# Performance work log

Measured on AMD Instinct MI355X. Metric: run time of the kernel, lower is better.

## Reference

```python
import jax, jax.numpy as jnp
import numpy as np

KEY_DIM, VALUE_DIM, NUM_HEAD, OUT_DIM = 128, 64, 4, 64
HEAD_KDIM = KEY_DIM // NUM_HEAD   # 32
HEAD_VDIM = VALUE_DIM // NUM_HEAD # 16

def _xavier(key, shape):
    # xavier_uniform over (fan_in=shape[0], fan_out=prod(shape[1:])) like torch
    fan_in, fan_out = shape[0], int(np.prod(shape[1:]))
    lim = float(np.sqrt(6.0 / (fan_in + fan_out)))
    return jax.random.uniform(key, shape, jnp.float32, -lim, lim)

def setup_inputs() -> dict:
    key = jax.random.key(0)
    ks = jax.random.split(key, 7)
    B, Q, K = 2, 4096, 4096
    return {
        "q_data": jax.random.normal(ks[0], (B, Q, KEY_DIM), jnp.float32),
        "m_data": jax.random.normal(ks[1], (B, K, VALUE_DIM), jnp.float32),
        "mask": jax.random.randint(ks[2], (B, K), 0, 2, jnp.int32),
        "q_weights": _xavier(ks[3], (KEY_DIM, NUM_HEAD, HEAD_KDIM)),
        "k_weights": _xavier(ks[4], (VALUE_DIM, NUM_HEAD, HEAD_KDIM)),
        "v_weights": _xavier(ks[5], (VALUE_DIM, NUM_HEAD, HEAD_VDIM)),
        "o_weights": _xavier(ks[6], (NUM_HEAD, HEAD_VDIM, OUT_DIM)),
        "o_bias": jnp.zeros((OUT_DIM,), jnp.float32),
    }

def reference(q_data, m_data, mask, q_weights, k_weights, v_weights, o_weights, o_bias):
    head_kdim = q_weights.shape[-1]
    scale = head_kdim ** (-0.5)
    Q = jnp.einsum('bqa,ahc->bqhc', q_data, q_weights) * scale
    K = jnp.einsum('bka,ahc->bkhc', m_data, k_weights)
    V = jnp.einsum('bka,ahc->bkhc', m_data, v_weights)
    logits = jnp.einsum('bqhc,bkhc->bhqk', Q, K)
    neg = jnp.finfo(logits.dtype).min
    logits = jnp.where(mask[:, None, None, :] == 0, neg, logits)
    weights = jax.nn.softmax(logits, axis=-1)
    weight_avg = jnp.einsum('bhqk,bkhc->bqhc', weights, V)
    return jnp.einsum('bqhc,hco->bqo', weight_avg, o_weights) + o_bias
```

## Files before the change

kernel.cpp:

```cpp
#include <hip/hip_runtime.h>
#include <stdint.h>

#define B_  2
#define QN  4096
#define KN  4096
#define AD  128
#define MD  64
#define H_  4
#define C_  32
#define CV  16
#define OD  64

typedef short bf16x8 __attribute__((ext_vector_type(8)));
typedef short bf16x4 __attribute__((ext_vector_type(4)));
typedef float f32x4  __attribute__((ext_vector_type(4)));

__device__ __forceinline__ short f2bf(float f) {
  union { float f; unsigned u; } v; v.f = f;
  unsigned r = v.u + 0x7fffu + ((v.u >> 16) & 1u);
  return (short)(r >> 16);
}
__device__ __forceinline__ unsigned pack2t(float a, float b) {
  union { float f; unsigned u; } ua, ub; ua.f = a; ub.f = b;
  return __builtin_amdgcn_perm(ub.u, ua.u, 0x07060302u);
}
__device__ __forceinline__ bf16x4 pack4t(f32x4 p) {
  union { unsigned u[2]; bf16x4 v; } t;
  t.u[0] = pack2t(p[0], p[1]); t.u[1] = pack2t(p[2], p[3]);
  return t.v;
}
__device__ __forceinline__ bf16x8 cvt8(f32x4 a, f32x4 b) {
  bf16x8 o;
  o[0]=f2bf(a[0]); o[1]=f2bf(a[1]); o[2]=f2bf(a[2]); o[3]=f2bf(a[3]);
  o[4]=f2bf(b[0]); o[5]=f2bf(b[1]); o[6]=f2bf(b[2]); o[7]=f2bf(b[3]);
  return o;
}

__global__ __launch_bounds__(256) void k_proj(const float* __restrict__ mdf,
                                              const float* __restrict__ kwf,
                                              const float* __restrict__ vwf,
                                              const int* __restrict__ mask, int* __restrict__ kc,
                                              short* __restrict__ Kp, short* __restrict__ Vpt) {
  __shared__ unsigned long long balS[64];
  __shared__ int pref[64];
  __shared__ int kcS;
  const int lane = threadIdx.x & 63;
  const int wid = threadIdx.x >> 6;
  const int n = lane & 15, quad = lane >> 4;
  const f32x4 z4 = {0.f,0.f,0.f,0.f};
  const int bidx = blockIdx.x;
  const int b = bidx / 768;
  #pragma unroll
  for (int p = 0; p < 16; ++p) {
    const int seg = wid*16 + p;
    const unsigned long long bal = __ballot(mask[b*KN + seg*64 + lane] != 0);
    if (lane == 0) balS[seg] = bal;
  }
  __syncthreads();
  if (wid == 0) {
    int v = __popcll(balS[lane]); int incl = v;
    for (int d = 1; d < 64; d <<= 1) { int o = __shfl_up(incl, d); if (lane >= d) incl += o; }
    pref[lane] = incl - v;
    if (lane == 63) kcS = incl;
  }
  __syncthreads();
  const int Kc = kcS;
  const int nch = (Kc + 31) >> 5;
  const int t = bidx*4 + wid;
  const int rem = t - b*3072;
  const int rt = rem / 12, ct = rem - rt*12;
  if (rem == 0 && lane == 0) kc[b] = Kc;
  if (rt*16 >= nch*32) return;
  const int j = rt*16 + n;
  const int valid = (j < Kc);
  int src = 0;
  if (valid) {
    int seg = 0;
    #pragma unroll
    for (int st = 32; st >= 1; st >>= 1)
      if (seg + st < 64 && pref[seg + st] <= j) seg += st;
    int r2 = j - pref[seg];
    unsigned long long m = balS[seg];
    int pos = 0;
    #pragma unroll
    for (int w = 32; w >= 1; w >>= 1) {
      const int c = __popcll(m & ((1ull << w) - 1ull));
      if (r2 >= c) { r2 -= c; m >>= w; pos += w; }
    }
    src = seg*64 + pos;
  }
  const float* mrow = mdf + (b*KN + src)*MD;
  const int hc = ct*16 + n;
  f32x4 acc = z4;
  #pragma unroll
  for (int ch = 0; ch < 2; ++ch) {
    const int a0 = ch*32 + quad*8;
    bf16x8 afrag = cvt8(*(const f32x4*)(mrow + a0), *(const f32x4*)(mrow + a0 + 4));
    if (!valid) {
      #pragma unroll
      for (int jj = 0; jj < 8; ++jj) afrag[jj] = 0;
    }
    bf16x8 bfrag;
    if (ct < 8) {
      #pragma unroll
      for (int jj = 0; jj < 8; ++jj) bfrag[jj] = f2bf(kwf[(a0 + jj)*128 + hc]);
    } else {
      #pragma unroll
      for (int jj = 0; jj < 8; ++jj) bfrag[jj] = f2bf(vwf[(a0 + jj)*64 + hc - 128]);
    }
    acc = __builtin_amdgcn_mfma_f32_16x16x32_bf16(afrag, bfrag, acc, 0, 0, 0);
  }
  if (ct < 8) {
    const int h = hc >> 5, c = hc & 31;
    #pragma unroll
    for (int r = 0; r < 4; ++r) {
      const int jj2 = rt*16 + quad*4 + r;
      Kp[((b*H_ + h)*KN + jj2)*C_ + c] = f2bf(acc[r]);
    }
  } else {
    const int hc2 = hc - 128; const int h = hc2 >> 4, cv = hc2 & 15;
    bf16x4 pk; pk[0]=f2bf(acc[0]); pk[1]=f2bf(acc[1]); pk[2]=f2bf(acc[2]); pk[3]=f2bf(acc[3]);
    *(bf16x4*)(Vpt + ((b*H_ + h)*CV + cv)*KN + rt*16 + quad*4) = pk;
  }
}

__global__ __launch_bounds__(1024) void k_attn(const float* __restrict__ qdf,
                                               const float* __restrict__ qwf,
                                               const short* __restrict__ Kp,
                                               const short* __restrict__ Vpt,
                                               const int* __restrict__ kc,
                                               const float* __restrict__ w2f,
                                               const float* __restrict__ obf,
                                               float* __restrict__ out) {
  __shared__ __attribute__((aligned(16))) char pool[40960];
  __shared__ __attribute__((aligned(16))) short QL[32*136];
  const int lane = threadIdx.x & 63, wid = threadIdx.x >> 6;
  const int h = wid & 3, split = wid >> 2;
  const int flatq = blockIdx.x * 32;
  const int b = flatq >> 12;
  const int bh = b*H_ + h;
  const int n = lane & 15, quad = lane >> 4;
  const int Kc = kc[b];
  const int nch = (Kc + 31) >> 5;
  const f32x4 z4 = {0.f,0.f,0.f,0.f};
  {
    const int mt = wid & 1, ct = wid >> 1;
    const int row = flatq + mt*16 + n;
    f32x4 acc = z4;
    #pragma unroll
    for (int ak = 0; ak < 4; ++ak) {
      const int a0 = ak*32 + quad*8;
      const float* ap = qdf + row*AD + a0;
      bf16x8 afrag = cvt8(*(const f32x4*)ap, *(const f32x4*)(ap + 4));
      bf16x8 bfrag;
      #pragma unroll
      for (int j = 0; j < 8; ++j) bfrag[j] = f2bf(qwf[(a0 + j)*128 + ct*16 + n]);
      acc = __builtin_amdgcn_mfma_f32_16x16x32_bf16(afrag, bfrag, acc, 0, 0, 0);
    }
    const float s = 0.17677669529663687f * 1.44269504088896341f;
    #pragma unroll
    for (int r = 0; r < 4; ++r)
      QL[(mt*16 + quad*4 + r)*136 + ct*16 + n] = f2bf(acc[r] * s);
  }
  __syncthreads();
  const bf16x8 qb0 = *(const bf16x8*)(QL + n*136 + h*32 + quad*8);
  const bf16x8 qb1 = *(const bf16x8*)(QL + (16 + n)*136 + h*32 + quad*8);
  const short* Kb = Kp + bh*KN*C_;
  const short* Vb = Vpt + bh*CV*KN;
  f32x4 o0 = z4, o1 = z4;
  float l0 = 0.f, l1 = 0.f;
  short* Pw = (short*)(pool + wid*2560);

  auto loadK = [&](int cc, bf16x8& f0, bf16x8& f1, bf16x8& v) {
    const int kb = cc*32;
    f0 = *(const bf16x8*)(Kb + (kb + n)*C_ + quad*8);
    f1 = *(const bf16x8*)(Kb + (kb + 16 + n)*C_ + quad*8);
    v  = *(const bf16x8*)(Vb + n*KN + kb + quad*8);
  };
  auto consume = [&](const bf16x8& ckf0, const bf16x8& ckf1, const bf16x8& cva) {
    f32x4 s00 = __builtin_amdgcn_mfma_f32_16x16x32_bf16(ckf0, qb0, z4, 0, 0, 0);
    f32x4 s01 = __builtin_amdgcn_mfma_f32_16x16x32_bf16(ckf0, qb1, z4, 0, 0, 0);
    f32x4 s10 = __builtin_amdgcn_mfma_f32_16x16x32_bf16(ckf1, qb0, z4, 0, 0, 0);
    f32x4 s11 = __builtin_amdgcn_mfma_f32_16x16x32_bf16(ckf1, qb1, z4, 0, 0, 0);
    f32x4 p00, p01, p10, p11;
    #pragma unroll
    for (int r = 0; r < 4; ++r) {
      p00[r] = __builtin_amdgcn_exp2f(s00[r]);
      p01[r] = __builtin_amdgcn_exp2f(s01[r]);
      p10[r] = __builtin_amdgcn_exp2f(s10[r]);
      p11[r] = __builtin_amdgcn_exp2f(s11[r]);
    }
    l0 += ((p00[0]+p00[1])+(p00[2]+p00[3])) + ((p10[0]+p10[1])+(p10[2]+p10[3]));
    l1 += ((p01[0]+p01[1])+(p01[2]+p01[3])) + ((p11[0]+p11[1])+(p11[2]+p11[3]));
    *(bf16x4*)(Pw + n*40 + quad*4)           = pack4t(p00);
    *(bf16x4*)(Pw + n*40 + 16 + quad*4)      = pack4t(p10);
    *(bf16x4*)(Pw + (16+n)*40 + quad*4)      = pack4t(p01);
    *(bf16x4*)(Pw + (16+n)*40 + 16 + quad*4) = pack4t(p11);
    const bf16x8 pb0 = *(const bf16x8*)(Pw + n*40 + quad*8);
    const bf16x8 pb1 = *(const bf16x8*)(Pw + (16+n)*40 + quad*8);
    o0 = __builtin_amdgcn_mfma_f32_16x16x32_bf16(cva, pb0, o0, 0, 0, 0);
    o1 = __builtin_amdgcn_mfma_f32_16x16x32_bf16(cva, pb1, o1, 0, 0, 0);
  };

  bf16x8 k00, k01, v0, k10, k11, v1, k20, k21, v2;
  int ci = split;
  if (ci < nch)     loadK(ci,     k00, k01, v0);
  if (ci + 4 < nch) loadK(ci + 4, k10, k11, v1);
  for (; ci < nch; ci += 12) {
    if (ci + 8 < nch) loadK(ci + 8, k20, k21, v2);
    consume(k00, k01, v0);
    if (ci + 4 < nch) {
      if (ci + 12 < nch) loadK(ci + 12, k00, k01, v0);
      consume(k10, k11, v1);
      if (ci + 8 < nch) {
        if (ci + 16 < nch) loadK(ci + 16, k10, k11, v1);
        consume(k20, k21, v2);
      }
    }
  }
  __syncthreads();
  float* Of   = (float*)pool;
  float* Lb   = (float*)(pool + 33280);
  short* ObfA = (short*)(pool + 35328);
  #pragma unroll
  for (int r = 0; r < 4; ++r) {
    const int hc = h*16 + quad*4 + r;
    Of[split*2080 + n*65 + hc]      = o0[r];
    Of[split*2080 + (16+n)*65 + hc] = o1[r];
  }
  l0 += __shfl_xor(l0, 16); l0 += __shfl_xor(l0, 32);
  l1 += __shfl_xor(l1, 16); l1 += __shfl_xor(l1, 32);
  if (lane < 16) {
    Lb[split*128 + h*32 + lane]      = l0;
    Lb[split*128 + h*32 + 16 + lane] = l1;
  }
  __syncthreads();
  {
    const float npad = (float)(nch*32 - Kc);
    const int e = threadIdx.x * 2;
    const int q = e >> 6, hc = e & 63;
    const int hh = hc >> 4;
    const float l = (Lb[hh*32 + q] + Lb[128 + hh*32 + q])
                  + (Lb[256 + hh*32 + q] + Lb[384 + hh*32 + q]) - npad;
    const float inv = 1.00135f / l;
    const float v0_ = ((Of[q*65 + hc]     + Of[2080 + q*65 + hc])
                     + (Of[4160 + q*65 + hc] + Of[6240 + q*65 + hc])) * inv;
    const float v1_ = ((Of[q*65 + hc + 1] + Of[2080 + q*65 + hc + 1])
                     + (Of[4160 + q*65 + hc + 1] + Of[6240 + q*65 + hc + 1])) * inv;
    union { unsigned u; short s[2]; } pk;
    pk.s[0] = f2bf(v0_); pk.s[1] = f2bf(v1_);
    *(unsigned*)(ObfA + q*72 + hc) = pk.u;
  }
  __syncthreads();
  if (wid < 8) {
    const int mt = wid & 1, nt = wid >> 1;
    f32x4 acc = z4;
    #pragma unroll
    for (int kchunk = 0; kchunk < 2; ++kchunk) {
      const bf16x8 afrag = *(const bf16x8*)(ObfA + (mt*16 + n)*72 + kchunk*32 + quad*8);
      bf16x8 bfrag;
      #pragma unroll
      for (int jj = 0; jj < 8; ++jj)
        bfrag[jj] = f2bf(w2f[(kchunk*32 + quad*8 + jj)*64 + nt*16 + n]);
      acc = __builtin_amdgcn_mfma_f32_16x16x32_bf16(afrag, bfrag, acc, 0, 0, 0);
    }
    const int ocol = nt*16 + n;
    const float bias = obf[ocol];
    #pragma unroll
    for (int r = 0; r < 4; ++r) {
      const int qg = flatq + mt*16 + quad*4 + r;
      out[qg*64 + ocol] = acc[r] + bias;
    }
  }
}

extern "C" void kernel_launch(void* const* d_in, const int* in_sizes, int n_in,
                              void* d_out, int out_size, void* d_ws, size_t ws_size,
                              hipStream_t stream) {
  const float* qd  = (const float*)d_in[0];
  const float* md  = (const float*)d_in[1];
  const int*   msk = (const int*)  d_in[2];
  const float* qw  = (const float*)d_in[3];
  const float* kw  = (const float*)d_in[4];
  const float* vw  = (const float*)d_in[5];
  const float* ow  = (const float*)d_in[6];
  const float* ob  = (const float*)d_in[7];
  float* out = (float*)d_out;

  char* ws = (char*)d_ws;
  int*   kc  = (int*)  (ws);
  short* Kp  = (short*)(ws + (64<<10));
  short* Vpt = (short*)(ws + (64<<10) + (2u<<20));

  hipLaunchKernelGGL(k_proj, dim3(1536), dim3(256),  0, stream, md, kw, vw, msk, kc, Kp, Vpt);
  hipLaunchKernelGGL(k_attn, dim3(256),  dim3(1024), 0, stream, qd, qw, Kp, Vpt, kc, ow, ob, out);
}
```

Before: 103.0 us.

## Software-pipeline QK/PV stages with double-buffered P and MFMA row sums

```diff
diff --git a/kernel.cpp b/kernel.cpp
--- a/kernel.cpp
+++ b/kernel.cpp
@@ -132,7 +132,7 @@
                                                const float* __restrict__ w2f,
                                                const float* __restrict__ obf,
                                                float* __restrict__ out) {
-  __shared__ __attribute__((aligned(16))) char pool[40960];
+  __shared__ __attribute__((aligned(16))) char pool[81920];
   __shared__ __attribute__((aligned(16))) short QL[32*136];
   const int lane = threadIdx.x & 63, wid = threadIdx.x >> 6;
   const int h = wid & 3, split = wid >> 2;
@@ -168,8 +168,12 @@
   const short* Kb = Kp + bh*KN*C_;
   const short* Vb = Vpt + bh*CV*KN;
   f32x4 o0 = z4, o1 = z4;
-  float l0 = 0.f, l1 = 0.f;
-  short* Pw = (short*)(pool + wid*2560);
+  f32x4 lacc0 = z4, lacc1 = z4;
+  short* Pw0 = (short*)(pool + wid*5120);
+  short* Pw1 = Pw0 + 1280;
+  bf16x8 onesv;
+  #pragma unroll
+  for (int j = 0; j < 8; ++j) onesv[j] = (short)0x3F80;
 
   auto loadK = [&](int cc, bf16x8& f0, bf16x8& f1, bf16x8& v) {
     const int kb = cc*32;
@@ -177,7 +181,7 @@
     f1 = *(const bf16x8*)(Kb + (kb + 16 + n)*C_ + quad*8);
     v  = *(const bf16x8*)(Vb + n*KN + kb + quad*8);
   };
-  auto consume = [&](const bf16x8& ckf0, const bf16x8& ckf1, const bf16x8& cva) {
+  auto stageA = [&](const bf16x8& ckf0, const bf16x8& ckf1, short* PwB) {
     f32x4 s00 = __builtin_amdgcn_mfma_f32_16x16x32_bf16(ckf0, qb0, z4, 0, 0, 0);
     f32x4 s01 = __builtin_amdgcn_mfma_f32_16x16x32_bf16(ckf0, qb1, z4, 0, 0, 0);
     f32x4 s10 = __builtin_amdgcn_mfma_f32_16x16x32_bf16(ckf1, qb0, z4, 0, 0, 0);
@@ -190,32 +194,41 @@
       p10[r] = __builtin_amdgcn_exp2f(s10[r]);
       p11[r] = __builtin_amdgcn_exp2f(s11[r]);
     }
-    l0 += ((p00[0]+p00[1])+(p00[2]+p00[3])) + ((p10[0]+p10[1])+(p10[2]+p10[3]));
-    l1 += ((p01[0]+p01[1])+(p01[2]+p01[3])) + ((p11[0]+p11[1])+(p11[2]+p11[3]));
-    *(bf16x4*)(Pw + n*40 + quad*4)           = pack4t(p00);
-    *(bf16x4*)(Pw + n*40 + 16 + quad*4)      = pack4t(p10);
-    *(bf16x4*)(Pw + (16+n)*40 + quad*4)      = pack4t(p01);
-    *(bf16x4*)(Pw + (16+n)*40 + 16 + quad*4) = pack4t(p11);
-    const bf16x8 pb0 = *(const bf16x8*)(Pw + n*40 + quad*8);
-    const bf16x8 pb1 = *(const bf16x8*)(Pw + (16+n)*40 + quad*8);
+    *(bf16x4*)(PwB + n*40 + quad*4)           = pack4t(p00);
+    *(bf16x4*)(PwB + n*40 + 16 + quad*4)      = pack4t(p10);
+    *(bf16x4*)(PwB + (16+n)*40 + quad*4)      = pack4t(p01);
+    *(bf16x4*)(PwB + (16+n)*40 + 16 + quad*4) = pack4t(p11);
+  };
+  auto stageB = [&](const bf16x8& cva, const short* PwB) {
+    const bf16x8 pb0 = *(const bf16x8*)(PwB + n*40 + quad*8);
+    const bf16x8 pb1 = *(const bf16x8*)(PwB + (16+n)*40 + quad*8);
     o0 = __builtin_amdgcn_mfma_f32_16x16x32_bf16(cva, pb0, o0, 0, 0, 0);
     o1 = __builtin_amdgcn_mfma_f32_16x16x32_bf16(cva, pb1, o1, 0, 0, 0);
+    lacc0 = __builtin_amdgcn_mfma_f32_16x16x32_bf16(onesv, pb0, lacc0, 0, 0, 0);
+    lacc1 = __builtin_amdgcn_mfma_f32_16x16x32_bf16(onesv, pb1, lacc1, 0, 0, 0);
   };
 
-  bf16x8 k00, k01, v0, k10, k11, v1, k20, k21, v2;
-  int ci = split;
-  if (ci < nch)     loadK(ci,     k00, k01, v0);
-  if (ci + 4 < nch) loadK(ci + 4, k10, k11, v1);
-  for (; ci < nch; ci += 12) {
-    if (ci + 8 < nch) loadK(ci + 8, k20, k21, v2);
-    consume(k00, k01, v0);
-    if (ci + 4 < nch) {
-      if (ci + 12 < nch) loadK(ci + 12, k00, k01, v0);
-      consume(k10, k11, v1);
-      if (ci + 8 < nch) {
-        if (ci + 16 < nch) loadK(ci + 16, k10, k11, v1);
-        consume(k20, k21, v2);
-      }
+  const int T = (nch > split) ? ((nch - split + 3) >> 2) : 0;
+  bf16x8 k00, k01, v0, k10, k11, v1;
+  if (T > 0) loadK(split,     k00, k01, v0);
+  if (T > 1) loadK(split + 4, k10, k11, v1);
+  if (T > 0) stageA(k00, k01, Pw0);
+  int c = 1;
+  for (; c + 1 < T; c += 2) {
+    stageB(v0, Pw0);
+    loadK(split + 4*(c+1), k00, k01, v0);
+    stageA(k10, k11, Pw1);
+    stageB(v1, Pw1);
+    if (c + 2 < T) loadK(split + 4*(c+2), k10, k11, v1);
+    stageA(k00, k01, Pw0);
+  }
+  if (T > 0) {
+    if (c == T) {
+      stageB(v0, Pw0);
+    } else {
+      stageB(v0, Pw0);
+      stageA(k10, k11, Pw1);
+      stageB(v1, Pw1);
     }
   }
   __syncthreads();
@@ -228,11 +241,9 @@
     Of[split*2080 + n*65 + hc]      = o0[r];
     Of[split*2080 + (16+n)*65 + hc] = o1[r];
   }
-  l0 += __shfl_xor(l0, 16); l0 += __shfl_xor(l0, 32);
-  l1 += __shfl_xor(l1, 16); l1 += __shfl_xor(l1, 32);
   if (lane < 16) {
-    Lb[split*128 + h*32 + lane]      = l0;
-    Lb[split*128 + h*32 + 16 + lane] = l1;
+    Lb[split*128 + h*32 + lane]      = lacc0[0];
+    Lb[split*128 + h*32 + 16 + lane] = lacc1[0];
   }
   __syncthreads();
   {
@@ -242,7 +253,7 @@
     const int hh = hc >> 4;
     const float l = (Lb[hh*32 + q] + Lb[128 + hh*32 + q])
                   + (Lb[256 + hh*32 + q] + Lb[384 + hh*32 + q]) - npad;
-    const float inv = 1.00135f / l;
+    const float inv = 1.0f / l;
     const float v0_ = ((Of[q*65 + hc]     + Of[2080 + q*65 + hc])
                      + (Of[4160 + q*65 + hc] + Of[6240 + q*65 + hc])) * inv;
     const float v1_ = ((Of[q*65 + hc + 1] + Of[2080 + q*65 + hc + 1])
```

Result: no change. 102.2 us (-0.8%).
